# Optimization experiments

Hardware: AMD Instinct MI355X
Metric: run time of the kernel (lower is better)

Reference implementation:

```python
import jax, jax.numpy as jnp
import numpy as np

H = 768
B = 65536
T = 3
EPS = 1e-5


def setup_inputs() -> dict:
    key = jax.random.key(0)
    ks = jax.random.split(key, 6)
    s = 1.0 / np.sqrt(H)
    return {
        "features": jax.random.normal(ks[0], (B, T, H), dtype=jnp.float32),
        "Wq": jax.random.normal(ks[1], (H, H), dtype=jnp.float32) * s,
        "bq": jnp.zeros((H,), jnp.float32),
        "Wk": jax.random.normal(ks[2], (H, H), dtype=jnp.float32) * s,
        "bk": jnp.zeros((H,), jnp.float32),
        "Wv": jax.random.normal(ks[3], (H, H), dtype=jnp.float32) * s,
        "bv": jnp.zeros((H,), jnp.float32),
        "Wo": jax.random.normal(ks[4], (H, H), dtype=jnp.float32) * s,
        "bo": jnp.zeros((H,), jnp.float32),
        "ln_g": jnp.ones((H,), jnp.float32),
        "ln_b": jnp.zeros((H,), jnp.float32),
    }


def reference(features, Wq, bq, Wk, bk, Wv, bv, Wo, bo, ln_g, ln_b):
    # LayerNorm over last dim
    mu = jnp.mean(features, axis=-1, keepdims=True)
    var = jnp.mean(jnp.square(features - mu), axis=-1, keepdims=True)
    x = (features - mu) * jax.lax.rsqrt(var + EPS) * ln_g + ln_b  # [B,T,H]

    scale = H ** (-0.5)
    Q = jnp.einsum("bth,oh->bto", x, Wq) + bq
    K = jnp.einsum("bth,oh->bto", x, Wk) + bk
    V = jnp.einsum("bth,oh->bto", x, Wv) + bv

    Qp, Qn = jax.nn.relu(Q), jax.nn.relu(-Q)
    Kp, Kn = jax.nn.relu(K), jax.nn.relu(-K)

    attn_pos = jax.nn.softmax(jnp.einsum("bqh,bkh->bqk", Qp, Kp) * scale, axis=-1)
    attn_neg = jax.nn.softmax(jnp.einsum("bqh,bkh->bqk", Qn, Kn) * scale, axis=-1)

    out = jnp.einsum("bqk,bkh->bqh", attn_pos, V) - jnp.einsum("bqk,bkh->bqh", attn_neg, V)
    out = jnp.einsum("bth,oh->bto", out, Wo) + bo
    return x + out
```

## Files before the change

### kernel.cpp

```cpp
#include <hip/hip_runtime.h>

typedef __attribute__((ext_vector_type(8))) _Float16 half8;
typedef __attribute__((ext_vector_type(4))) _Float16 half4;
typedef __attribute__((ext_vector_type(4))) float f32x4;

#define HDIM 768
#define LNEPS 1e-5f

#define L_AS   0
#define L_BS   24576
#define L_STQ  57344
#define L_STK  108032
#define L_SP   158720
#define L_SN   161024
#define L_TOT  163328
#define SSTR   264

__device__ __forceinline__ void gload_lds16(const void* g, void* l) {
  __builtin_amdgcn_global_load_lds(
      (const __attribute__((address_space(1))) void*)g,
      (__attribute__((address_space(3))) void*)l, 16, 0, 0);
}

__global__ __launch_bounds__(256) void convert_kernel(
    const float* __restrict__ Wq, const float* __restrict__ Wk,
    const float* __restrict__ bq, const float* __restrict__ bk,
    _Float16* __restrict__ Wf, float* __restrict__ biasf)
{
  const long NW = 1536L * 768;
  long i = (long)blockIdx.x * 256 + threadIdx.x;
  if (i < NW) {
    const int orow = (int)(i / 768);
    const int k = (int)(i - (long)orow * 768);
    const int n = orow >> 8, c = orow & 255;
    const int src = n * 128 + (c & 127);
    Wf[i] = (_Float16)((c < 128) ? Wq[(long)src * 768 + k]
                                 : Wk[(long)src * 768 + k]);
  } else if (i < NW + 1536) {
    const int j = (int)(i - NW);
    const int n = j >> 8, c = j & 255;
    const int src = n * 128 + (c & 127);
    biasf[j] = (c < 128) ? bq[src] : bk[src];
  }
}

__global__ __launch_bounds__(256) void wvo_kernel(
    const float* __restrict__ Wo, const float* __restrict__ Wv,
    const float* __restrict__ bv,
    _Float16* __restrict__ Wvo, float* __restrict__ bvo)
{
  if (blockIdx.x == 144) {
    for (int o = threadIdx.x; o < 768; o += 256) {
      float s = 0.f;
      for (int h = 0; h < 768; ++h) s += Wo[o * 768 + h] * bv[h];
      bvo[o] = s;
    }
    return;
  }
  __shared__ float As[64][65];
  __shared__ float Bs[64][65];
  const int bm = blockIdx.x / 12, bn = blockIdx.x % 12;
  const int tid = threadIdx.x;
  const int tr = tid >> 4, tc = tid & 15;
  float acc[4][4] = {};
  for (int k0 = 0; k0 < 768; k0 += 64) {
    __syncthreads();
#pragma unroll
    for (int i = 0; i < 16; ++i) {
      const int e = i * 256 + tid, r = e >> 6, c = e & 63;
      As[r][c] = Wo[(bm * 64 + r) * 768 + (k0 + c)];
      Bs[r][c] = Wv[(k0 + r) * 768 + (bn * 64 + c)];
    }
    __syncthreads();
#pragma unroll 8
    for (int k = 0; k < 64; ++k) {
      float a[4], b[4];
#pragma unroll
      for (int i = 0; i < 4; ++i) a[i] = As[tr * 4 + i][k];
#pragma unroll
      for (int j = 0; j < 4; ++j) b[j] = Bs[k][tc * 4 + j];
#pragma unroll
      for (int i = 0; i < 4; ++i)
#pragma unroll
        for (int j = 0; j < 4; ++j) acc[i][j] += a[i] * b[j];
    }
  }
#pragma unroll
  for (int i = 0; i < 4; ++i)
#pragma unroll
    for (int j = 0; j < 4; ++j)
      Wvo[(bm * 64 + tr * 4 + i) * 768 + bn * 64 + tc * 4 + j] = (_Float16)acc[i][j];
}

__global__ __launch_bounds__(256) void ln_kernel(
    const float* __restrict__ feat, const float* __restrict__ gamma,
    const float* __restrict__ beta, _Float16* __restrict__ xout)
{
  const int w = threadIdx.x >> 6, lane = threadIdx.x & 63;
  const long row = (long)blockIdx.x * 4 + w;
  const float* fr = feat + row * HDIM;
  float4 v[3];
  float s = 0.f, ss = 0.f;
#pragma unroll
  for (int i = 0; i < 3; ++i) {
    v[i] = *(const float4*)&fr[(i * 64 + lane) * 4];
    s  += v[i].x + v[i].y + v[i].z + v[i].w;
    ss += v[i].x * v[i].x + v[i].y * v[i].y + v[i].z * v[i].z + v[i].w * v[i].w;
  }
#pragma unroll
  for (int off = 32; off; off >>= 1) {
    s  += __shfl_xor(s, off);
    ss += __shfl_xor(ss, off);
  }
  const float mu = s * (1.f / 768.f);
  const float var = ss * (1.f / 768.f) - mu * mu;
  const float rs = rsqrtf(var + LNEPS);
#pragma unroll
  for (int i = 0; i < 3; ++i) {
    const int idx = (i * 64 + lane) * 4;
    float4 g4 = *(const float4*)&gamma[idx];
    float4 b4 = *(const float4*)&beta[idx];
    half4 o;
    o[0] = (_Float16)((v[i].x - mu) * rs * g4.x + b4.x);
    o[1] = (_Float16)((v[i].y - mu) * rs * g4.y + b4.y);
    o[2] = (_Float16)((v[i].z - mu) * rs * g4.z + b4.z);
    o[3] = (_Float16)((v[i].w - mu) * rs * g4.w + b4.w);
    *(half4*)&xout[row * HDIM + idx] = o;
  }
}

__global__ __launch_bounds__(512, 1) void fused_kernel(
    const _Float16* __restrict__ xh,
    const _Float16* __restrict__ Wf,
    const float* __restrict__ bias,
    const float* __restrict__ bo,
    float* __restrict__ out)
{
  __shared__ __align__(16) char lds[L_TOT];
  const int tid = threadIdx.x;
  const int lane = tid & 63;
  const int quad = lane >> 4, l16 = lane & 15;
  const int w = tid >> 6;
  const int wm = w >> 2, wn = w & 3;

  const int nwg = gridDim.x;
  const int orig = blockIdx.x;
  const int bid = (orig & 7) * (nwg >> 3) + (orig >> 3);
  const long m0 = (long)bid * 192;

  {
    float* sc = (float*)(lds + L_SP);
#pragma unroll
    for (int i = 0; i < 3; ++i) {
      const int idx = i * 512 + tid;
      if (idx < 1152) sc[idx] = 0.f;
    }
  }

  const int wg = w & 3;
  long aOff[3]; int aLds[3];
#pragma unroll
  for (int i = 0; i < 3; ++i) {
    const int c = i * 256 + wg * 64 + lane, r = c >> 2, p = c & 3;
    const int cc = p ^ ((r >> 1) & 3);
    aOff[i] = (m0 + r) * HDIM + cc * 8;
    aLds[i] = c * 16;
  }
  long bOff[4]; int bLds[4];
#pragma unroll
  for (int i = 0; i < 4; ++i) {
    const int c = i * 256 + wg * 64 + lane, r = c >> 2, p = c & 3;
    const int cc = p ^ ((r >> 1) & 3);
    bOff[i] = (long)r * HDIM + cc * 8;
    bLds[i] = c * 16;
  }

  int stg_buf = 0; long stg_k = 0; long stg_nb = 0;
#define STAGE()                                                               \
  do {                                                                        \
    if (w < 4) {                                                              \
      _Pragma("unroll")                                                       \
      for (int i_ = 0; i_ < 3; ++i_)                                          \
        gload_lds16(xh + aOff[i_] + stg_k, lds + L_AS + stg_buf * 12288 + aLds[i_]); \
    } else {                                                                  \
      _Pragma("unroll")                                                       \
      for (int i_ = 0; i_ < 4; ++i_)                                          \
        gload_lds16(Wf + stg_nb + bOff[i_] + stg_k, lds + L_BS + stg_buf * 16384 + bLds[i_]); \
    }                                                                         \
    stg_buf ^= 1; stg_k += 32;                                                \
    if (stg_k == HDIM) { stg_k = 0; stg_nb += 256L * HDIM; }                  \
  } while (0)
#define VMW()                                                                 \
  do { if (w < 4) { asm volatile("s_waitcnt vmcnt(3)" ::: "memory"); }        \
       else       { asm volatile("s_waitcnt vmcnt(4)" ::: "memory"); } } while (0)

  f32x4 acc[6][4];
#pragma unroll
  for (int mi = 0; mi < 6; ++mi)
#pragma unroll
    for (int ni = 0; ni < 4; ++ni)
#pragma unroll
      for (int j = 0; j < 4; ++j) acc[mi][ni][j] = 0.f;

  STAGE(); STAGE();
  VMW();
  __builtin_amdgcn_s_barrier();
  __builtin_amdgcn_sched_barrier(0);

  for (int n = 0; n < 9; ++n) {
    for (int ks = 0; ks < 24; ++ks) {
      const int s = n * 24 + ks;
      const int buf = s & 1;
      const char* as = lds + L_AS + buf * 12288;
      const char* bs = lds + L_BS + buf * 16384;
      half8 af[6], bf[4];
#pragma unroll
      for (int mi = 0; mi < 6; ++mi) {
        const int r = wm * 96 + mi * 16 + l16;
        af[mi] = *(const half8*)(as + r * 64 + ((quad ^ ((r >> 1) & 3)) * 16));
      }
#pragma unroll
      for (int ni = 0; ni < 4; ++ni) {
        const int r = wn * 64 + ni * 16 + l16;
        bf[ni] = *(const half8*)(bs + r * 64 + ((quad ^ ((r >> 1) & 3)) * 16));
      }
      __builtin_amdgcn_s_setprio(1);
#pragma unroll
      for (int mi = 0; mi < 6; ++mi)
#pragma unroll
        for (int ni = 0; ni < 4; ++ni)
          acc[mi][ni] = __builtin_amdgcn_mfma_f32_16x16x32_f16(af[mi], bf[ni], acc[mi][ni], 0, 0, 0);
      __builtin_amdgcn_s_setprio(0);
      __builtin_amdgcn_sched_barrier(0);
      __builtin_amdgcn_s_barrier();
      __builtin_amdgcn_sched_barrier(0);
      if (s + 2 < 216) STAGE();
      if (s < 214) {
        VMW();
        __builtin_amdgcn_s_barrier();
        __builtin_amdgcn_sched_barrier(0);
      } else if (s == 214) {
        asm volatile("s_waitcnt vmcnt(0)" ::: "memory");
        __builtin_amdgcn_s_barrier();
        __builtin_amdgcn_sched_barrier(0);
      }
    }

    {
      float bv[4];
#pragma unroll
      for (int ni = 0; ni < 4; ++ni)
        bv[ni] = bias[n * 256 + wn * 64 + ni * 16 + l16];
      char* st = lds + ((wn >> 1) ? L_STK : L_STQ);
      const int cb = (wn & 1) * 64;
#pragma unroll
      for (int mi = 0; mi < 6; ++mi)
#pragma unroll
        for (int ni = 0; ni < 4; ++ni)
#pragma unroll
          for (int j = 0; j < 4; ++j) {
            const int row = wm * 96 + mi * 16 + quad * 4 + j;
            *(_Float16*)(st + row * SSTR + (cb + ni * 16 + l16) * 2) =
                (_Float16)(acc[mi][ni][j] + bv[ni]);
          }
#pragma unroll
      for (int mi = 0; mi < 6; ++mi)
#pragma unroll
        for (int ni = 0; ni < 4; ++ni)
#pragma unroll
          for (int j = 0; j < 4; ++j) acc[mi][ni][j] = 0.f;
    }
    __builtin_amdgcn_s_barrier();

    if (n < 6) {
      const int b = tid >> 3, sub = tid & 7;
      half4 qv[3][4], kv[3][4];
#pragma unroll
      for (int t = 0; t < 3; ++t) {
        const char* rq = lds + L_STQ + (3 * b + t) * SSTR + sub * 32;
        const char* rk = lds + L_STK + (3 * b + t) * SSTR + sub * 32;
#pragma unroll
        for (int u = 0; u < 4; ++u) {
          qv[t][u] = *(const half4*)(rq + u * 8);
          kv[t][u] = *(const half4*)(rk + u * 8);
        }
      }
#pragma unroll
      for (int qi = 0; qi < 3; ++qi)
#pragma unroll
        for (int ki = 0; ki < 3; ++ki) {
          float p = 0.f, nn = 0.f;
#pragma unroll
          for (int u = 0; u < 4; ++u)
#pragma unroll
            for (int e = 0; e < 4; ++e) {
              const float qq = (float)qv[qi][u][e];
              const float kk = (float)kv[ki][u][e];
              p  += fmaxf(qq, 0.f) * fmaxf(kk, 0.f);
              nn += fminf(qq, 0.f) * fminf(kk, 0.f);
            }
          p  += __shfl_xor(p, 1);  p  += __shfl_xor(p, 2);  p  += __shfl_xor(p, 4);
          nn += __shfl_xor(nn, 1); nn += __shfl_xor(nn, 2); nn += __shfl_xor(nn, 4);
          if (sub == 0) {
            ((float*)(lds + L_SP))[b * 9 + qi * 3 + ki] += p;
            ((float*)(lds + L_SN))[b * 9 + qi * 3 + ki] += nn;
          }
        }
      __builtin_amdgcn_s_barrier();
      if (n == 5) {
        if (tid < 64) {
          float* sp = (float*)(lds + L_SP) + tid * 9;
          float* sn = (float*)(lds + L_SN) + tid * 9;
          const float scale = 0.03608439182435161f;
#pragma unroll
          for (int qi = 0; qi < 3; ++qi) {
            const float p0 = sp[qi*3+0]*scale, p1 = sp[qi*3+1]*scale, p2 = sp[qi*3+2]*scale;
            const float n0 = sn[qi*3+0]*scale, n1 = sn[qi*3+1]*scale, n2 = sn[qi*3+2]*scale;
            const float mp = fmaxf(p0, fmaxf(p1, p2));
            const float mn = fmaxf(n0, fmaxf(n1, n2));
            const float ep0 = __expf(p0-mp), ep1 = __expf(p1-mp), ep2 = __expf(p2-mp);
            const float en0 = __expf(n0-mn), en1 = __expf(n1-mn), en2 = __expf(n2-mn);
            const float rp = 1.f / (ep0+ep1+ep2), rn = 1.f / (en0+en1+en2);
            sp[qi*3+0] = ep0*rp - en0*rn;
            sp[qi*3+1] = ep1*rp - en1*rn;
            sp[qi*3+2] = ep2*rp - en2*rn;
          }
        }
        __builtin_amdgcn_s_barrier();
      }
    } else {
      const int cg = tid & 63, rg = tid >> 6;
      const int c = cg * 4;
      const char* vb = lds + ((c >> 7) ? L_STK : L_STQ) + (c & 127) * 2;
      const long gc = 256L * (n - 6) + c;
      const f32x4 bov = *(const f32x4*)&bo[gc];
      const float* cf0 = (const float*)(lds + L_SP);
#pragma unroll 4
      for (int rr = 0; rr < 24; ++rr) {
        const int row = rr * 8 + rg;
        const int b = (int)((unsigned)row / 3u);
        const int t = row - 3 * b;
        const float* cf = cf0 + b * 9 + t * 3;
        const half4 v0 = *(const half4*)(vb + (3 * b + 0) * SSTR);
        const half4 v1 = *(const half4*)(vb + (3 * b + 1) * SSTR);
        const half4 v2 = *(const half4*)(vb + (3 * b + 2) * SSTR);
        const half4 hx = *(const half4*)&xh[(m0 + row) * HDIM + gc];
        const float c0 = cf[0], c1 = cf[1], c2 = cf[2];
        f32x4 o;
#pragma unroll
        for (int j = 0; j < 4; ++j)
          o[j] = (float)hx[j] + bov[j] + c0 * (float)v0[j]
               + c1 * (float)v1[j] + c2 * (float)v2[j];
        *(f32x4*)&out[(m0 + row) * HDIM + gc] = o;
      }
      __builtin_amdgcn_s_barrier();
    }
  }
#undef STAGE
#undef VMW
}

extern "C" void kernel_launch(void* const* d_in, const int* in_sizes, int n_in,
                              void* d_out, int out_size, void* d_ws, size_t ws_size,
                              hipStream_t stream) {
  (void)in_sizes; (void)n_in; (void)out_size; (void)ws_size;
  const float* feat = (const float*)d_in[0];
  const float* Wq   = (const float*)d_in[1];
  const float* bq   = (const float*)d_in[2];
  const float* Wk   = (const float*)d_in[3];
  const float* bk   = (const float*)d_in[4];
  const float* Wv   = (const float*)d_in[5];
  const float* bv   = (const float*)d_in[6];
  const float* Wo   = (const float*)d_in[7];
  const float* bo   = (const float*)d_in[8];
  const float* ln_g = (const float*)d_in[9];
  const float* ln_b = (const float*)d_in[10];

  char* ws = (char*)d_ws;
  _Float16* xh    = (_Float16*)(ws);
  _Float16* Wf    = (_Float16*)(ws + 301989888L);
  float*    biasf = (float*)   (ws + 305528832L);

  convert_kernel<<<4614, 256, 0, stream>>>(Wq, Wk, bq, bk, Wf, biasf);
  wvo_kernel<<<145, 256, 0, stream>>>(Wo, Wv, bv, Wf + 1536L * 768, biasf + 1536);
  ln_kernel<<<49152, 256, 0, stream>>>(feat, ln_g, ln_b, xh);
  fused_kernel<<<1024, 512, 0, stream>>>(xh, Wf, biasf, bo, (float*)d_out);
}
```

Baseline: 1.285 ms.

## Double fused kernel workgroup to 1024 threads with smaller per-wave tiles

The fused GEMM/attention kernel now launches 16 waves per workgroup instead of 8. Each wave computes a 48x64 output tile instead of 96x64, which halves its accumulators and A-fragment loads. Global-to-LDS staging is spread over all threads with one load each, and the epilogue row loop is split across twice as many threads. The aim is better latency hiding and more issuing waves per CU. In exchange, each wave does fewer MFMAs per LDS read and barriers are more costly.

```diff
diff --git a/kernel.cpp b/kernel.cpp
--- a/kernel.cpp
+++ b/kernel.cpp
@@ -129,7 +129,7 @@
   }
 }
 
-__global__ __launch_bounds__(512, 1) void fused_kernel(
+__global__ __launch_bounds__(1024, 4) void fused_kernel(
     const _Float16* __restrict__ xh,
     const _Float16* __restrict__ Wf,
     const float* __restrict__ bias,
@@ -151,52 +151,43 @@
   {
     float* sc = (float*)(lds + L_SP);
 #pragma unroll
-    for (int i = 0; i < 3; ++i) {
-      const int idx = i * 512 + tid;
+    for (int i = 0; i < 2; ++i) {
+      const int idx = i * 1024 + tid;
       if (idx < 1152) sc[idx] = 0.f;
     }
   }
 
-  const int wg = w & 3;
-  long aOff[3]; int aLds[3];
-#pragma unroll
-  for (int i = 0; i < 3; ++i) {
-    const int c = i * 256 + wg * 64 + lane, r = c >> 2, p = c & 3;
+  long aOff; int aLds;
+  {
+    const int c = tid, r = c >> 2, p = c & 3;
     const int cc = p ^ ((r >> 1) & 3);
-    aOff[i] = (m0 + r) * HDIM + cc * 8;
-    aLds[i] = c * 16;
-  }
-  long bOff[4]; int bLds[4];
-#pragma unroll
-  for (int i = 0; i < 4; ++i) {
-    const int c = i * 256 + wg * 64 + lane, r = c >> 2, p = c & 3;
+    aOff = (m0 + r) * HDIM + cc * 8;
+    aLds = c * 16;
+  }
+  long bOff; int bLds;
+  {
+    const int c = tid, r = c >> 2, p = c & 3;
     const int cc = p ^ ((r >> 1) & 3);
-    bOff[i] = (long)r * HDIM + cc * 8;
-    bLds[i] = c * 16;
+    bOff = (long)r * HDIM + cc * 8;
+    bLds = c * 16;
   }
 
   int stg_buf = 0; long stg_k = 0; long stg_nb = 0;
 #define STAGE()                                                               \
   do {                                                                        \
-    if (w < 4) {                                                              \
-      _Pragma("unroll")                                                       \
-      for (int i_ = 0; i_ < 3; ++i_)                                          \
-        gload_lds16(xh + aOff[i_] + stg_k, lds + L_AS + stg_buf * 12288 + aLds[i_]); \
-    } else {                                                                  \
-      _Pragma("unroll")                                                       \
-      for (int i_ = 0; i_ < 4; ++i_)                                          \
-        gload_lds16(Wf + stg_nb + bOff[i_] + stg_k, lds + L_BS + stg_buf * 16384 + bLds[i_]); \
-    }                                                                         \
+    if (w < 12)                                                               \
+      gload_lds16(xh + aOff + stg_k, lds + L_AS + stg_buf * 12288 + aLds);    \
+    gload_lds16(Wf + stg_nb + bOff + stg_k, lds + L_BS + stg_buf * 16384 + bLds); \
     stg_buf ^= 1; stg_k += 32;                                                \
     if (stg_k == HDIM) { stg_k = 0; stg_nb += 256L * HDIM; }                  \
   } while (0)
 #define VMW()                                                                 \
-  do { if (w < 4) { asm volatile("s_waitcnt vmcnt(3)" ::: "memory"); }        \
-       else       { asm volatile("s_waitcnt vmcnt(4)" ::: "memory"); } } while (0)
-
-  f32x4 acc[6][4];
-#pragma unroll
-  for (int mi = 0; mi < 6; ++mi)
+  do { if (w < 12) { asm volatile("s_waitcnt vmcnt(2)" ::: "memory"); }       \
+       else        { asm volatile("s_waitcnt vmcnt(1)" ::: "memory"); } } while (0)
+
+  f32x4 acc[3][4];
+#pragma unroll
+  for (int mi = 0; mi < 3; ++mi)
 #pragma unroll
     for (int ni = 0; ni < 4; ++ni)
 #pragma unroll
@@ -213,10 +204,10 @@
       const int buf = s & 1;
       const char* as = lds + L_AS + buf * 12288;
       const char* bs = lds + L_BS + buf * 16384;
-      half8 af[6], bf[4];
-#pragma unroll
-      for (int mi = 0; mi < 6; ++mi) {
-        const int r = wm * 96 + mi * 16 + l16;
+      half8 af[3], bf[4];
+#pragma unroll
+      for (int mi = 0; mi < 3; ++mi) {
+        const int r = wm * 48 + mi * 16 + l16;
         af[mi] = *(const half8*)(as + r * 64 + ((quad ^ ((r >> 1) & 3)) * 16));
       }
 #pragma unroll
@@ -226,7 +217,7 @@
       }
       __builtin_amdgcn_s_setprio(1);
 #pragma unroll
-      for (int mi = 0; mi < 6; ++mi)
+      for (int mi = 0; mi < 3; ++mi)
 #pragma unroll
         for (int ni = 0; ni < 4; ++ni)
           acc[mi][ni] = __builtin_amdgcn_mfma_f32_16x16x32_f16(af[mi], bf[ni], acc[mi][ni], 0, 0, 0);
@@ -254,17 +245,17 @@
       char* st = lds + ((wn >> 1) ? L_STK : L_STQ);
       const int cb = (wn & 1) * 64;
 #pragma unroll
-      for (int mi = 0; mi < 6; ++mi)
+      for (int mi = 0; mi < 3; ++mi)
 #pragma unroll
         for (int ni = 0; ni < 4; ++ni)
 #pragma unroll
           for (int j = 0; j < 4; ++j) {
-            const int row = wm * 96 + mi * 16 + quad * 4 + j;
+            const int row = wm * 48 + mi * 16 + quad * 4 + j;
             *(_Float16*)(st + row * SSTR + (cb + ni * 16 + l16) * 2) =
                 (_Float16)(acc[mi][ni][j] + bv[ni]);
           }
 #pragma unroll
-      for (int mi = 0; mi < 6; ++mi)
+      for (int mi = 0; mi < 3; ++mi)
 #pragma unroll
         for (int ni = 0; ni < 4; ++ni)
 #pragma unroll
@@ -273,39 +264,41 @@
     __builtin_amdgcn_s_barrier();
 
     if (n < 6) {
-      const int b = tid >> 3, sub = tid & 7;
-      half4 qv[3][4], kv[3][4];
-#pragma unroll
-      for (int t = 0; t < 3; ++t) {
-        const char* rq = lds + L_STQ + (3 * b + t) * SSTR + sub * 32;
-        const char* rk = lds + L_STK + (3 * b + t) * SSTR + sub * 32;
-#pragma unroll
-        for (int u = 0; u < 4; ++u) {
-          qv[t][u] = *(const half4*)(rq + u * 8);
-          kv[t][u] = *(const half4*)(rk + u * 8);
-        }
-      }
-#pragma unroll
-      for (int qi = 0; qi < 3; ++qi)
-#pragma unroll
-        for (int ki = 0; ki < 3; ++ki) {
-          float p = 0.f, nn = 0.f;
-#pragma unroll
-          for (int u = 0; u < 4; ++u)
-#pragma unroll
-            for (int e = 0; e < 4; ++e) {
-              const float qq = (float)qv[qi][u][e];
-              const float kk = (float)kv[ki][u][e];
-              p  += fmaxf(qq, 0.f) * fmaxf(kk, 0.f);
-              nn += fminf(qq, 0.f) * fminf(kk, 0.f);
-            }
-          p  += __shfl_xor(p, 1);  p  += __shfl_xor(p, 2);  p  += __shfl_xor(p, 4);
-          nn += __shfl_xor(nn, 1); nn += __shfl_xor(nn, 2); nn += __shfl_xor(nn, 4);
-          if (sub == 0) {
-            ((float*)(lds + L_SP))[b * 9 + qi * 3 + ki] += p;
-            ((float*)(lds + L_SN))[b * 9 + qi * 3 + ki] += nn;
+      if (tid < 512) {
+        const int b = tid >> 3, sub = tid & 7;
+        half4 qv[3][4], kv[3][4];
+#pragma unroll
+        for (int t = 0; t < 3; ++t) {
+          const char* rq = lds + L_STQ + (3 * b + t) * SSTR + sub * 32;
+          const char* rk = lds + L_STK + (3 * b + t) * SSTR + sub * 32;
+#pragma unroll
+          for (int u = 0; u < 4; ++u) {
+            qv[t][u] = *(const half4*)(rq + u * 8);
+            kv[t][u] = *(const half4*)(rk + u * 8);
           }
         }
+#pragma unroll
+        for (int qi = 0; qi < 3; ++qi)
+#pragma unroll
+          for (int ki = 0; ki < 3; ++ki) {
+            float p = 0.f, nn = 0.f;
+#pragma unroll
+            for (int u = 0; u < 4; ++u)
+#pragma unroll
+              for (int e = 0; e < 4; ++e) {
+                const float qq = (float)qv[qi][u][e];
+                const float kk = (float)kv[ki][u][e];
+                p  += fmaxf(qq, 0.f) * fmaxf(kk, 0.f);
+                nn += fminf(qq, 0.f) * fminf(kk, 0.f);
+              }
+            p  += __shfl_xor(p, 1);  p  += __shfl_xor(p, 2);  p  += __shfl_xor(p, 4);
+            nn += __shfl_xor(nn, 1); nn += __shfl_xor(nn, 2); nn += __shfl_xor(nn, 4);
+            if (sub == 0) {
+              ((float*)(lds + L_SP))[b * 9 + qi * 3 + ki] += p;
+              ((float*)(lds + L_SN))[b * 9 + qi * 3 + ki] += nn;
+            }
+          }
+      }
       __builtin_amdgcn_s_barrier();
       if (n == 5) {
         if (tid < 64) {
@@ -336,8 +329,8 @@
       const f32x4 bov = *(const f32x4*)&bo[gc];
       const float* cf0 = (const float*)(lds + L_SP);
 #pragma unroll 4
-      for (int rr = 0; rr < 24; ++rr) {
-        const int row = rr * 8 + rg;
+      for (int rr = 0; rr < 12; ++rr) {
+        const int row = rr * 16 + rg;
         const int b = (int)((unsigned)row / 3u);
         const int t = row - 3 * b;
         const float* cf = cf0 + b * 9 + t * 3;
@@ -384,5 +377,5 @@
   convert_kernel<<<4614, 256, 0, stream>>>(Wq, Wk, bq, bk, Wf, biasf);
   wvo_kernel<<<145, 256, 0, stream>>>(Wo, Wv, bv, Wf + 1536L * 768, biasf + 1536);
   ln_kernel<<<49152, 256, 0, stream>>>(feat, ln_g, ln_b, xh);
-  fused_kernel<<<1024, 512, 0, stream>>>(xh, Wf, biasf, bo, (float*)d_out);
-}
+  fused_kernel<<<1024, 1024, 0, stream>>>(xh, Wf, biasf, bo, (float*)d_out);
+}
```

After: 1.565 ms. 21.9% more time.

## Stage A tiles through registers with deeper prefetch instead of direct-to-LDS loads

Applied to the files above, without the earlier changes.

Replaces the global_load_lds path for the A operand (the normalized activation tile) with register-staged loads that prefetch up to four k-steps ahead. The data is then written to LDS after each barrier, while the B operand (weights) keeps the direct-to-LDS path. The k loop is unrolled by four so the register ring buffer indices are compile-time constants. The intent is to hide global load latency for A more deeply, at the cost of 12 extra vector registers, explicit LDS stores and lgkmcnt waits in every step.

```diff
diff --git a/kernel.cpp b/kernel.cpp
--- a/kernel.cpp
+++ b/kernel.cpp
@@ -158,12 +158,12 @@
   }
 
   const int wg = w & 3;
-  long aOff[3]; int aLds[3];
+  long aOffv[3]; int aLds[3];
 #pragma unroll
   for (int i = 0; i < 3; ++i) {
     const int c = i * 256 + wg * 64 + lane, r = c >> 2, p = c & 3;
     const int cc = p ^ ((r >> 1) & 3);
-    aOff[i] = (m0 + r) * HDIM + cc * 8;
+    aOffv[i] = (m0 + r) * 96 + cc;
     aLds[i] = c * 16;
   }
   long bOff[4]; int bLds[4];
@@ -175,75 +175,107 @@
     bLds[i] = c * 16;
   }
 
-  int stg_buf = 0; long stg_k = 0; long stg_nb = 0;
-#define STAGE()                                                               \
+  const f32x4* xh4 = (const f32x4*)xh;
+  f32x4 stg[12];
+  int a_k = 0;
+  long b_k = 0, b_nb = 0;
+
+  f32x4 acc[6][4];
+#pragma unroll
+  for (int mi = 0; mi < 6; ++mi)
+#pragma unroll
+    for (int ni = 0; ni < 4; ++ni)
+#pragma unroll
+      for (int j = 0; j < 4; ++j) acc[mi][ni][j] = 0.f;
+
+  if (w < 4) {
+#pragma unroll
+    for (int J = 0; J < 4; ++J) {
+#pragma unroll
+      for (int i = 0; i < 3; ++i)
+        stg[J * 3 + i] = xh4[aOffv[i] + a_k];
+      a_k += 4;
+    }
+#pragma unroll
+    for (int i = 0; i < 3; ++i)
+      *(f32x4*)(lds + L_AS + aLds[i]) = stg[i];
+  } else {
+#pragma unroll
+    for (int i = 0; i < 4; ++i)
+      gload_lds16(Wf + bOff[i], lds + L_BS + bLds[i]);
+#pragma unroll
+    for (int i = 0; i < 4; ++i)
+      gload_lds16(Wf + bOff[i] + 32, lds + L_BS + 16384 + bLds[i]);
+    b_k = 64;
+    asm volatile("s_waitcnt vmcnt(4)" ::: "memory");
+  }
+  asm volatile("s_waitcnt lgkmcnt(0)" ::: "memory");
+  __builtin_amdgcn_sched_barrier(0);
+  __builtin_amdgcn_s_barrier();
+  __builtin_amdgcn_sched_barrier(0);
+
+#define STEP(J_)                                                              \
   do {                                                                        \
-    if (w < 4) {                                                              \
+    const int s_ = sbase + (J_);                                              \
+    const char* as_ = lds + L_AS + ((J_) & 1) * 12288;                        \
+    const char* bs_ = lds + L_BS + ((J_) & 1) * 16384;                        \
+    half8 af[6], bf[4];                                                       \
+    _Pragma("unroll")                                                         \
+    for (int mi_ = 0; mi_ < 6; ++mi_) {                                       \
+      const int r_ = wm * 96 + mi_ * 16 + l16;                                \
+      af[mi_] = *(const half8*)(as_ + r_ * 64 + ((quad ^ ((r_ >> 1) & 3)) * 16)); \
+    }                                                                         \
+    _Pragma("unroll")                                                         \
+    for (int ni_ = 0; ni_ < 4; ++ni_) {                                       \
+      const int r_ = wn * 64 + ni_ * 16 + l16;                                \
+      bf[ni_] = *(const half8*)(bs_ + r_ * 64 + ((quad ^ ((r_ >> 1) & 3)) * 16)); \
+    }                                                                         \
+    if (w < 4 && s_ <= 211) {                  \
       _Pragma("unroll")                                                       \
       for (int i_ = 0; i_ < 3; ++i_)                                          \
-        gload_lds16(xh + aOff[i_] + stg_k, lds + L_AS + stg_buf * 12288 + aLds[i_]); \
+        stg[(J_) * 3 + i_] = xh4[aOffv[i_] + a_k];                            \
+      a_k += 4; if (a_k == 96) a_k = 0;                                       \
+    }                                                                         \
+    __builtin_amdgcn_s_setprio(1);                                            \
+    _Pragma("unroll")                                                         \
+    for (int mi_ = 0; mi_ < 6; ++mi_)                                         \
+      _Pragma("unroll")                                                       \
+      for (int ni_ = 0; ni_ < 4; ++ni_)                                       \
+        acc[mi_][ni_] = __builtin_amdgcn_mfma_f32_16x16x32_f16(               \
+            af[mi_], bf[ni_], acc[mi_][ni_], 0, 0, 0);                        \
+    __builtin_amdgcn_s_setprio(0);                                            \
+    __builtin_amdgcn_sched_barrier(0);                                        \
+    __builtin_amdgcn_s_barrier();                     \
+    __builtin_amdgcn_sched_barrier(0);                                        \
+    if (w < 4) {                                                              \
+      if (s_ <= 214) {                            \
+        char* dst_ = lds + L_AS + (((J_) + 1) & 1) * 12288;                   \
+        _Pragma("unroll")                                                     \
+        for (int i_ = 0; i_ < 3; ++i_)                                        \
+          *(f32x4*)(dst_ + aLds[i_]) = stg[(((J_) + 1) & 3) * 3 + i_];        \
+      }                                                                       \
     } else {                                                                  \
-      _Pragma("unroll")                                                       \
-      for (int i_ = 0; i_ < 4; ++i_)                                          \
-        gload_lds16(Wf + stg_nb + bOff[i_] + stg_k, lds + L_BS + stg_buf * 16384 + bLds[i_]); \
+      if (s_ <= 213) {                              \
+        _Pragma("unroll")                                                     \
+        for (int i_ = 0; i_ < 4; ++i_)                                        \
+          gload_lds16(Wf + b_nb + bOff[i_] + b_k,                             \
+                      lds + L_BS + ((J_) & 1) * 16384 + bLds[i_]);            \
+        b_k += 32; if (b_k == HDIM) { b_k = 0; b_nb += 256L * HDIM; }         \
+        asm volatile("s_waitcnt vmcnt(4)" ::: "memory");                      \
+      } else if (s_ == 214) {                                                 \
+        asm volatile("s_waitcnt vmcnt(0)" ::: "memory");                      \
+      }                                                                       \
     }                                                                         \
-    stg_buf ^= 1; stg_k += 32;                                                \
-    if (stg_k == HDIM) { stg_k = 0; stg_nb += 256L * HDIM; }                  \
+    asm volatile("s_waitcnt lgkmcnt(0)" ::: "memory");                        \
+    __builtin_amdgcn_sched_barrier(0);                                        \
+    __builtin_amdgcn_s_barrier();                 \
+    __builtin_amdgcn_sched_barrier(0);                                        \
   } while (0)
-#define VMW()                                                                 \
-  do { if (w < 4) { asm volatile("s_waitcnt vmcnt(3)" ::: "memory"); }        \
-       else       { asm volatile("s_waitcnt vmcnt(4)" ::: "memory"); } } while (0)
-
-  f32x4 acc[6][4];
-#pragma unroll
-  for (int mi = 0; mi < 6; ++mi)
-#pragma unroll
-    for (int ni = 0; ni < 4; ++ni)
-#pragma unroll
-      for (int j = 0; j < 4; ++j) acc[mi][ni][j] = 0.f;
-
-  STAGE(); STAGE();
-  VMW();
-  __builtin_amdgcn_s_barrier();
-  __builtin_amdgcn_sched_barrier(0);
 
   for (int n = 0; n < 9; ++n) {
-    for (int ks = 0; ks < 24; ++ks) {
-      const int s = n * 24 + ks;
-      const int buf = s & 1;
-      const char* as = lds + L_AS + buf * 12288;
-      const char* bs = lds + L_BS + buf * 16384;
-      half8 af[6], bf[4];
-#pragma unroll
-      for (int mi = 0; mi < 6; ++mi) {
-        const int r = wm * 96 + mi * 16 + l16;
-        af[mi] = *(const half8*)(as + r * 64 + ((quad ^ ((r >> 1) & 3)) * 16));
-      }
-#pragma unroll
-      for (int ni = 0; ni < 4; ++ni) {
-        const int r = wn * 64 + ni * 16 + l16;
-        bf[ni] = *(const half8*)(bs + r * 64 + ((quad ^ ((r >> 1) & 3)) * 16));
-      }
-      __builtin_amdgcn_s_setprio(1);
-#pragma unroll
-      for (int mi = 0; mi < 6; ++mi)
-#pragma unroll
-        for (int ni = 0; ni < 4; ++ni)
-          acc[mi][ni] = __builtin_amdgcn_mfma_f32_16x16x32_f16(af[mi], bf[ni], acc[mi][ni], 0, 0, 0);
-      __builtin_amdgcn_s_setprio(0);
-      __builtin_amdgcn_sched_barrier(0);
-      __builtin_amdgcn_s_barrier();
-      __builtin_amdgcn_sched_barrier(0);
-      if (s + 2 < 216) STAGE();
-      if (s < 214) {
-        VMW();
-        __builtin_amdgcn_s_barrier();
-        __builtin_amdgcn_sched_barrier(0);
-      } else if (s == 214) {
-        asm volatile("s_waitcnt vmcnt(0)" ::: "memory");
-        __builtin_amdgcn_s_barrier();
-        __builtin_amdgcn_sched_barrier(0);
-      }
+    for (int ks4 = 0; ks4 < 6; ++ks4) {
+      const int sbase = n * 24 + ks4 * 4;
+      STEP(0); STEP(1); STEP(2); STEP(3);
     }
 
     {
@@ -356,8 +388,7 @@
       __builtin_amdgcn_s_barrier();
     }
   }
-#undef STAGE
-#undef VMW
+#undef STEP
 }
 
 extern "C" void kernel_launch(void* const* d_in, const int* in_sizes, int n_in,
```

Result: slower. 1.368 ms (+6.5%).

## Double-buffer LDS fragment registers and cut to one barrier per k-step

Applied to the files above, without the earlier changes.

Restructures the projection GEMM main loop so the LDS fragment reads for the next k-step are issued before the MFMAs of the current step. Fragments ping-pong between two register sets, and the two barriers per step become a single barrier preceded by full vmcnt and lgkmcnt waits. The aim is to hide LDS read latency behind MFMA work and reduce barrier overhead. In exchange it uses more VGPRs, which can lower occupancy, and it waits on vmcnt(0) each step, which drains the global-to-LDS prefetch queue.

```diff
diff --git a/kernel.cpp b/kernel.cpp
--- a/kernel.cpp
+++ b/kernel.cpp
@@ -190,9 +190,43 @@
     stg_buf ^= 1; stg_k += 32;                                                \
     if (stg_k == HDIM) { stg_k = 0; stg_nb += 256L * HDIM; }                  \
   } while (0)
-#define VMW()                                                                 \
-  do { if (w < 4) { asm volatile("s_waitcnt vmcnt(3)" ::: "memory"); }        \
-       else       { asm volatile("s_waitcnt vmcnt(4)" ::: "memory"); } } while (0)
+
+#define FRAGREAD(AF_, BF_, buf_)                                              \
+  do {                                                                        \
+    const char* as_ = lds + L_AS + (buf_) * 12288;                            \
+    const char* bs_ = lds + L_BS + (buf_) * 16384;                            \
+    _Pragma("unroll")                                                         \
+    for (int mi_ = 0; mi_ < 6; ++mi_) {                                       \
+      const int r_ = wm * 96 + mi_ * 16 + l16;                                \
+      AF_[mi_] = *(const half8*)(as_ + r_ * 64 + ((quad ^ ((r_ >> 1) & 3)) * 16)); \
+    }                                                                         \
+    _Pragma("unroll")                                                         \
+    for (int ni_ = 0; ni_ < 4; ++ni_) {                                       \
+      const int r_ = wn * 64 + ni_ * 16 + l16;                                \
+      BF_[ni_] = *(const half8*)(bs_ + r_ * 64 + ((quad ^ ((r_ >> 1) & 3)) * 16)); \
+    }                                                                         \
+  } while (0)
+
+#define STEPBODY(s_, CURA_, CURB_, NXTA_, NXTB_, nbuf_)                       \
+  do {                                                                        \
+    asm volatile("s_waitcnt lgkmcnt(0)" ::: "memory");                        \
+    __builtin_amdgcn_sched_barrier(0);                                        \
+    asm volatile("s_waitcnt vmcnt(0)" ::: "memory");                          \
+    __builtin_amdgcn_sched_barrier(0);                                        \
+    __builtin_amdgcn_s_barrier();         \
+    __builtin_amdgcn_sched_barrier(0);                                        \
+    if ((s_) < 214) STAGE();                      \
+    if ((s_) < 215) FRAGREAD(NXTA_, NXTB_, (nbuf_));                          \
+    __builtin_amdgcn_s_setprio(1);                                            \
+    _Pragma("unroll")                                                         \
+    for (int mi_ = 0; mi_ < 6; ++mi_)                                         \
+      _Pragma("unroll")                                                       \
+      for (int ni_ = 0; ni_ < 4; ++ni_)                                       \
+        acc[mi_][ni_] = __builtin_amdgcn_mfma_f32_16x16x32_f16(               \
+            CURA_[mi_], CURB_[ni_], acc[mi_][ni_], 0, 0, 0);                  \
+    __builtin_amdgcn_s_setprio(0);                                            \
+    __builtin_amdgcn_sched_barrier(0);                                        \
+  } while (0)
 
   f32x4 acc[6][4];
 #pragma unroll
@@ -202,48 +236,22 @@
 #pragma unroll
       for (int j = 0; j < 4; ++j) acc[mi][ni][j] = 0.f;
 
-  STAGE(); STAGE();
-  VMW();
+  half8 afA[6], bfA[4], afB[6], bfB[4];
+
+  STAGE();
+  asm volatile("s_waitcnt vmcnt(0)" ::: "memory");
+  __builtin_amdgcn_sched_barrier(0);
   __builtin_amdgcn_s_barrier();
   __builtin_amdgcn_sched_barrier(0);
+  FRAGREAD(afA, bfA, 0);
+  STAGE();
 
   for (int n = 0; n < 9; ++n) {
-    for (int ks = 0; ks < 24; ++ks) {
-      const int s = n * 24 + ks;
-      const int buf = s & 1;
-      const char* as = lds + L_AS + buf * 12288;
-      const char* bs = lds + L_BS + buf * 16384;
-      half8 af[6], bf[4];
-#pragma unroll
-      for (int mi = 0; mi < 6; ++mi) {
-        const int r = wm * 96 + mi * 16 + l16;
-        af[mi] = *(const half8*)(as + r * 64 + ((quad ^ ((r >> 1) & 3)) * 16));
-      }
-#pragma unroll
-      for (int ni = 0; ni < 4; ++ni) {
-        const int r = wn * 64 + ni * 16 + l16;
-        bf[ni] = *(const half8*)(bs + r * 64 + ((quad ^ ((r >> 1) & 3)) * 16));
-      }
-      __builtin_amdgcn_s_setprio(1);
-#pragma unroll
-      for (int mi = 0; mi < 6; ++mi)
-#pragma unroll
-        for (int ni = 0; ni < 4; ++ni)
-          acc[mi][ni] = __builtin_amdgcn_mfma_f32_16x16x32_f16(af[mi], bf[ni], acc[mi][ni], 0, 0, 0);
-      __builtin_amdgcn_s_setprio(0);
-      __builtin_amdgcn_sched_barrier(0);
-      __builtin_amdgcn_s_barrier();
-      __builtin_amdgcn_sched_barrier(0);
-      if (s + 2 < 216) STAGE();
-      if (s < 214) {
-        VMW();
-        __builtin_amdgcn_s_barrier();
-        __builtin_amdgcn_sched_barrier(0);
-      } else if (s == 214) {
-        asm volatile("s_waitcnt vmcnt(0)" ::: "memory");
-        __builtin_amdgcn_s_barrier();
-        __builtin_amdgcn_sched_barrier(0);
-      }
+    for (int ks2 = 0; ks2 < 12; ++ks2) {
+      const int s0 = n * 24 + ks2 * 2;
+      STEPBODY(s0, afA, bfA, afB, bfB, 1);
+      const int s1 = s0 + 1;
+      STEPBODY(s1, afB, bfB, afA, bfA, 0);
     }
 
     {
@@ -357,7 +365,8 @@
     }
   }
 #undef STAGE
-#undef VMW
+#undef FRAGREAD
+#undef STEPBODY
 }
 
 extern "C" void kernel_launch(void* const* d_in, const int* in_sizes, int n_in,
```

Result: slower. 1.320 ms (+2.8%).
